# Kernel optimization log

Measured on AMD Instinct MI355X. Metric: run time of the kernel, lower is better.

The kernel has to match this reference:

```python
import jax, jax.numpy as jnp
import numpy as np

IMAGE_W = 1024
IMAGE_H = 1024
STRIDES = (8, 16, 32, 64, 128)
TOP_N = 1000
MIN_SCORE = 0.05
NMS_THR = 0.6
MAX_DET = 100
NEG = -1e9  # sentinel for suppressed scores


def _positions(stride):
    # Faithful to repo: shifts_x indexed by feature_h, shifts_y by feature_w,
    # grid built [hf, wf, 2] = [shift_x_i, shift_y_j], then permute(1,0,2).
    hf, wf = IMAGE_H // stride, IMAGE_W // stride
    sx = (jnp.arange(hf, dtype=jnp.float32) + 0.5) * stride
    sy = (jnp.arange(wf, dtype=jnp.float32) + 0.5) * stride
    pos = jnp.stack(jnp.meshgrid(sx, sy, indexing='ij'), axis=-1)  # [hf, wf, 2]
    return jnp.transpose(pos, (1, 0, 2)).reshape(-1, 2)  # [hf*wf, 2]


def _filter_level(cls_h, reg_h, ctr_h, pos):
    B, C = cls_h.shape[0], cls_h.shape[-1]
    cls_h = jax.nn.sigmoid(cls_h).reshape(B, -1, C)
    reg_h = jnp.exp(reg_h).reshape(B, -1, 4)
    ctr_h = jax.nn.sigmoid(ctr_h).reshape(B, -1)
    scores = jnp.max(cls_h, axis=-1)
    classes = jnp.argmax(cls_h, axis=-1).astype(jnp.int32)
    scores = jnp.sqrt(scores * ctr_h)
    N = scores.shape[1]
    if N >= TOP_N:
        scores, idx = jax.lax.top_k(scores, TOP_N)  # sorted descending, like torch.topk
        classes = jnp.take_along_axis(classes, idx, axis=1)
        reg_h = jnp.take_along_axis(reg_h, idx[..., None], axis=1)
        posb = pos[idx]  # [B, TOP_N, 2]
    else:
        posb = jnp.broadcast_to(pos[None], (B, N, 2))
    return scores, classes, reg_h, posb


def _snap(reg, pos):
    # reg: [B, N, 4] (l,t,r,b), pos: [B, N, 2]
    b = jnp.concatenate([pos - reg[:, :, 0:2], pos + reg[:, :, 2:4]], axis=-1)
    b = b.astype(jnp.int32)  # torch .int() truncation
    b = jnp.stack([
        jnp.maximum(b[..., 0], 0),
        jnp.maximum(b[..., 1], 0),
        jnp.minimum(b[..., 2], IMAGE_W - 1),
        jnp.minimum(b[..., 3], IMAGE_H - 1),
    ], axis=-1)
    return b.astype(jnp.float32)


def _nms_image(scores, classes, boxes):
    # scores [N], classes [N] int32, boxes [N,4] float (already snapped to int grid)
    s = jnp.where(scores > MIN_SCORE, scores, NEG)
    x1, y1, x2, y2 = boxes[:, 0], boxes[:, 1], boxes[:, 2], boxes[:, 3]
    areas = (x2 - x1) * (y2 - y1)
    out_s = -jnp.ones((MAX_DET,), jnp.float32)
    out_c = -jnp.ones((MAX_DET,), jnp.float32)
    out_b = -jnp.ones((MAX_DET, 4), jnp.float32)

    def body(i, st):
        s, os_, oc, ob = st
        idx = jnp.argmax(s)            # highest remaining score -> sorted keep order
        ok = s[idx] > MIN_SCORE        # any un-suppressed valid candidate left?
        bb = boxes[idx]
        iw = jnp.clip(jnp.minimum(x2, bb[2]) - jnp.maximum(x1, bb[0]), 0.0)
        ih = jnp.clip(jnp.minimum(y2, bb[3]) - jnp.maximum(y1, bb[1]), 0.0)
        inter = iw * ih
        iou = inter / (areas + areas[idx] - inter + 1e-12)
        s = jnp.where((iou > NMS_THR) & ok, NEG, s)
        s = s.at[idx].set(NEG)
        os_ = os_.at[i].set(jnp.where(ok, scores[idx], -1.0))
        oc = oc.at[i].set(jnp.where(ok, classes[idx].astype(jnp.float32), -1.0))
        ob = ob.at[i].set(jnp.where(ok, bb, -jnp.ones((4,), jnp.float32)))
        return (s, os_, oc, ob)

    _, os_, oc, ob = jax.lax.fori_loop(0, MAX_DET, body, (s, out_s, out_c, out_b))
    return os_, oc, ob


def _decode(cls_heads, reg_heads, ctr_heads):
    sc_l, cl_l, rg_l, ps_l = [], [], [], []
    for c, r, t, st in zip(cls_heads, reg_heads, ctr_heads, STRIDES):
        sc, cl, rg, ps = _filter_level(c, r, t, _positions(st))
        sc_l.append(sc); cl_l.append(cl); rg_l.append(rg); ps_l.append(ps)
    scores = jnp.concatenate(sc_l, axis=1)
    classes = jnp.concatenate(cl_l, axis=1)
    regs = jnp.concatenate(rg_l, axis=1)
    poss = jnp.concatenate(ps_l, axis=1)
    boxes = _snap(regs, poss)
    return jax.vmap(_nms_image)(scores, classes, boxes)


def setup_inputs() -> dict:
    key = jax.random.key(0)
    ks = jax.random.split(key, 15)
    B, C = 8, 80
    sizes = [IMAGE_H // s for s in STRIDES]
    inp = {}
    for i, hw in enumerate(sizes):
        inp[f'cls{i}'] = jax.random.normal(ks[i], (B, hw, hw, C), dtype=jnp.float32)
        # +3 so exp(reg) gives realistic ~20px extents
        inp[f'reg{i}'] = jax.random.normal(ks[5 + i], (B, hw, hw, 4), dtype=jnp.float32) + 3.0
        inp[f'ctr{i}'] = jax.random.normal(ks[10 + i], (B, hw, hw, 1), dtype=jnp.float32)
    return inp


def reference(cls0, cls1, cls2, cls3, cls4,
              reg0, reg1, reg2, reg3, reg4,
              ctr0, ctr1, ctr2, ctr3, ctr4):
    cls_heads = [cls0, cls1, cls2, cls3, cls4]
    reg_heads = [reg0, reg1, reg2, reg3, reg4]
    ctr_heads = [ctr0, ctr1, ctr2, ctr3, ctr4]
    batch_scores, batch_classes, batch_boxes = _decode(cls_heads, reg_heads, ctr_heads)
    return batch_scores, batch_classes, batch_boxes
```

## Files before the change

### kernel.cpp

```cpp
#include <hip/hip_runtime.h>

#define NPOS 21824
#define MINS 0.05f
#define BT   1024
#define NW   (BT/64)
#define TFAST 0.85f
#define CAP  16384
#define CNTSTRIDE 32

struct Ptrs { const float* cls[5]; const float* reg[5]; const float* ctr[5]; };

__device__ __forceinline__ float sigf(float x){ return 1.0f/(1.0f+expf(-x)); }

__device__ __forceinline__ unsigned long long mkkey(unsigned int b, int p){
    return ((unsigned long long)b << 16) | (unsigned)(65535 - p);
}

__device__ __forceinline__ float4 computeBox(const Ptrs& P, int img, int p){
    int base, lw, stride, lvl;
    if (p < 16384)      { lvl=0; base=0;     lw=7; stride=8;   }
    else if (p < 20480) { lvl=1; base=16384; lw=6; stride=16;  }
    else if (p < 21504) { lvl=2; base=20480; lw=5; stride=32;  }
    else if (p < 21760) { lvl=3; base=21504; lw=4; stride=64;  }
    else                { lvl=4; base=21760; lw=3; stride=128; }
    int pl = p - base;
    int h = pl >> lw, w = pl & ((1<<lw)-1);
    long long lidx = (long long)img*(1<<(2*lw)) + pl;
    float4 rg = ((const float4*)P.reg[lvl])[lidx];
    float x = (w + 0.5f)*(float)stride;
    float y = (h + 0.5f)*(float)stride;
    int ix1 = (int)(x - expf(rg.x));
    int iy1 = (int)(y - expf(rg.y));
    int ix2 = (int)(x + expf(rg.z));
    int iy2 = (int)(y + expf(rg.w));
    ix1 = max(ix1,0); iy1 = max(iy1,0);
    ix2 = min(ix2,1023); iy2 = min(iy2,1023);
    return make_float4((float)ix1,(float)iy1,(float)ix2,(float)iy2);
}

__global__ __launch_bounds__(256) void k_score(Ptrs P, float* scoreAll, int* clsAll,
                                               unsigned long long* list, int* listCnt)
{
    __shared__ int lcnt, lbase;
    int img  = blockIdx.y;
    int blk  = blockIdx.x;
    int tid  = threadIdx.x;
    int posb = tid >> 2;
    int l    = tid & 3;
    int p    = blk*64 + posb;
    int lvl, base, lw;
    if (blk < 256)      { lvl=0; base=0;     lw=7; }
    else if (blk < 320) { lvl=1; base=16384; lw=6; }
    else if (blk < 336) { lvl=2; base=20480; lw=5; }
    else if (blk < 340) { lvl=3; base=21504; lw=4; }
    else                { lvl=4; base=21760; lw=3; }
    int pl = p - base;
    long long lidx = (long long)img*(1<<(2*lw)) + pl;

    if (tid == 0) lcnt = 0;
    __syncthreads();

    const float4* c4 = (const float4*)(P.cls[lvl] + lidx*80);
    float mx = -3.4e38f; int mi = 0;
#pragma unroll
    for (int j = 0; j < 5; ++j) {
        int k = j*4 + l;
        float4 v = c4[k];
        int cb = k*4;
        if (v.x > mx){mx=v.x; mi=cb;}
        if (v.y > mx){mx=v.y; mi=cb+1;}
        if (v.z > mx){mx=v.z; mi=cb+2;}
        if (v.w > mx){mx=v.w; mi=cb+3;}
    }
#pragma unroll
    for (int d = 1; d < 4; d <<= 1) {
        float omx = __shfl_xor(mx, d);
        int   omi = __shfl_xor(mi, d);
        if (omx > mx || (omx == mx && omi < mi)) { mx = omx; mi = omi; }
    }
    int myTicket = -1;
    unsigned long long myKey = 0;
    if (l == 0) {
        float ct = P.ctr[lvl][lidx];
        float sc = sqrtf(sigf(mx)*sigf(ct));
        int o = img*NPOS + p;
        scoreAll[o] = sc;
        clsAll[o]   = mi;
        if (sc > TFAST) {
            myTicket = atomicAdd(&lcnt, 1);
            myKey = mkkey(__float_as_uint(sc), p);
        }
    }
    __syncthreads();
    if (tid == 0) lbase = lcnt ? atomicAdd(&listCnt[img*CNTSTRIDE], lcnt) : 0;
    __syncthreads();
    if (myTicket >= 0) {
        int t = lbase + myTicket;
        if (t < CAP) list[(long long)img*CAP + t] = myKey;
    }
}

__device__ void suffix_pick(const int* hist, int* wsum, int K,
                            unsigned int prefBase, int shift,
                            unsigned int* shPref, int* shK, int tid)
{
    int lo = tid*2;
    int h0 = hist[lo], h1 = hist[lo+1];
    int ls = h0 + h1;
    int lane = tid & 63, wv = tid >> 6;
    int v = ls;
#pragma unroll
    for (int off = 1; off < 64; off <<= 1) {
        int o = __shfl_down(v, off);
        if (lane + off < 64) v += o;
    }
    if (lane == 0) wsum[wv] = v;
    __syncthreads();
    int add = 0;
    for (int q = wv + 1; q < NW; ++q) add += wsum[q];
    int mine = v + add;
    int above = mine - ls;
    if (above < K && mine >= K) {
        if (above + h1 >= K) { *shPref = prefBase | ((unsigned)(lo+1) << shift); *shK = K - above; }
        else                 { *shPref = prefBase | ((unsigned)lo << shift); *shK = K - above - h1; }
    }
    __syncthreads();
}

__global__ __launch_bounds__(BT) void k_nms(Ptrs P, const float* scoreAll,
                                            const int* clsAll,
                                            const unsigned long long* list,
                                            const int* listCnt, float* out)
{
    __shared__ int histA[2048], histB[2048], wsum[NW];
    __shared__ unsigned int shPref;
    __shared__ int shK, tick, eqn;
    __shared__ unsigned long long eqKey[1024];
    __shared__ unsigned long long sel[256];
    __shared__ unsigned long long sorted[256];
    __shared__ float4 sBox[256];
    __shared__ float  sCls[256];
    __shared__ __align__(16) unsigned long long sRow[256][4];
    __shared__ int accIdx[100];
    __shared__ float4 accBox[100];
    __shared__ int shNaM, shNa;
    __shared__ unsigned long long shLast;

    int img = blockIdx.x, tid = threadIdx.x;
    const unsigned int* gs = (const unsigned int*)scoreAll + (long long)img*NPOS;
    const int* gCls = clsAll + (long long)img*NPOS;
    const unsigned long long* gl = list + (long long)img*CAP;

    float* outS = out + img*100;
    float* outC = out + 800 + img*100;
    float* outB = out + 1600 + img*400;

    int cnt = listCnt[img*CNTSTRIDE];
    bool fastPath = (cnt >= 256 && cnt <= CAP);

    for (int i = tid; i < 2048; i += BT) { histA[i] = 0; histB[i] = 0; }
    if (tid == 0) { tick = 0; eqn = 0; }
    __syncthreads();

    unsigned int kth; int need;
    if (fastPath) {
        for (int i = tid; i < cnt; i += BT)
            atomicAdd(&histA[(unsigned)(gl[i] >> 35)], 1);
        __syncthreads();
        suffix_pick(histA, wsum, 256, 0u, 19, &shPref, &shK, tid);
        unsigned int pref = shPref; int K2 = shK;
        for (int i = tid; i < cnt; i += BT) {
            unsigned long long k = gl[i];
            if ((unsigned)(k >> 35) == (pref >> 19))
                atomicAdd(&histB[(unsigned)(k >> 24) & 2047], 1);
        }
        __syncthreads();
        suffix_pick(histB, wsum, K2, pref, 8, &shPref, &shK, tid);
        kth = shPref >> 8; need = shK;
        for (int i = tid; i < cnt; i += BT) {
            unsigned long long k = gl[i];
            unsigned int hb = (unsigned)(k >> 24);
            if (hb > kth)       { int t = atomicAdd(&tick, 1); sel[t] = k; }
            else if (hb == kth) { int t = atomicAdd(&eqn, 1); if (t < 1024) eqKey[t] = k; }
        }
    } else {
#pragma unroll 4
        for (int i = tid; i < NPOS; i += BT)
            atomicAdd(&histA[gs[i] >> 19], 1);
        __syncthreads();
        suffix_pick(histA, wsum, 256, 0u, 19, &shPref, &shK, tid);
        unsigned int pref = shPref; int K2 = shK;
#pragma unroll 4
        for (int i = tid; i < NPOS; i += BT) {
            unsigned int b = gs[i];
            if ((b >> 19) == (pref >> 19)) atomicAdd(&histB[(b >> 8) & 2047], 1);
        }
        __syncthreads();
        suffix_pick(histB, wsum, K2, pref, 8, &shPref, &shK, tid);
        kth = shPref >> 8; need = shK;
#pragma unroll 4
        for (int i = tid; i < NPOS; i += BT) {
            unsigned int b = gs[i], hb = b >> 8;
            if (hb > kth)       { int t = atomicAdd(&tick, 1); sel[t] = mkkey(b, i); }
            else if (hb == kth) { int t = atomicAdd(&eqn, 1); if (t < 1024) eqKey[t] = mkkey(b, i); }
        }
    }
    __syncthreads();
    int m = eqn, nG = tick;
    if (m <= 1024) {
        for (int q = tid; q < m; q += BT) {
            unsigned long long kq = eqKey[q];
            int r = 0;
            for (int j = 0; j < m; ++j) r += (eqKey[j] > kq);
            if (r < need) sel[nG + r] = kq;
        }
    } else if (tid == 0) {
        unsigned long long last = ~0ULL;
        for (int c = 0; c < need; ++c) {
            unsigned long long best = 0;
            if (fastPath) {
                for (int i = 0; i < cnt; ++i) {
                    unsigned long long k2 = gl[i];
                    if ((unsigned)(k2 >> 24) == kth && k2 < last && k2 > best) best = k2;
                }
            } else {
                for (int i = 0; i < NPOS; ++i) {
                    unsigned int b = gs[i];
                    if ((b >> 8) == kth) {
                        unsigned long long k2 = mkkey(b, i);
                        if (k2 < last && k2 > best) best = k2;
                    }
                }
            }
            sel[nG + c] = best; last = best;
        }
    }
    __syncthreads();

    if (tid < 256) {
        unsigned long long k = sel[tid];
        int r = 0;
        for (int j = 0; j < 256; ++j) r += (sel[j] > k);
        sorted[r] = k;
    }
    __syncthreads();
    if (tid < 256) {
        int p = 65535 - (int)(sorted[tid] & 0xFFFF);
        sBox[tid] = computeBox(P, img, p);
        sCls[tid] = (float)gCls[p];
    }

    float myScore = 0.f;
    if (tid < 256) myScore = __uint_as_float((unsigned int)(sorted[tid] >> 16));
    int nValid = __syncthreads_count(myScore > MINS ? 1 : 0);

    {
        int row = tid & 255, qq = tid >> 8;
        float4 bi = sBox[row];
        float  ai = (bi.z-bi.x)*(bi.w-bi.y);
        unsigned long long mv = 0;
#pragma unroll 8
        for (int jj = 0; jj < 64; ++jj) {
            int j = qq*64 + jj;
            float4 bj = sBox[j];
            float aj = (bj.z-bj.x)*(bj.w-bj.y);
            float iw = fmaxf(fminf(bj.z,bi.z)-fmaxf(bj.x,bi.x),0.f);
            float ih = fmaxf(fminf(bj.w,bi.w)-fmaxf(bj.y,bi.y),0.f);
            float in_ = iw*ih;
            bool s = (j > row) && (in_/(aj+ai-in_+1e-12f) > 0.6f);
            mv |= ((unsigned long long)s) << jj;
        }
        sRow[row][qq] = mv;
    }
    __syncthreads();

    if (tid == 0) {
        int na = 0;
        unsigned long long r0=0, r1=0, r2=0, r3=0;
#define FCOS_WBLK(RW, IB)                                                  \
        {                                                                  \
            int hi = nValid < ((IB)+1)*64 ? nValid : ((IB)+1)*64;          \
            for (int i = (IB)*64; i < hi && na < 100; ++i) {               \
                if ((RW >> (i - (IB)*64)) & 1ull) continue;                \
                accIdx[na++] = i;                                          \
                const ulonglong2* rp = (const ulonglong2*)sRow[i];         \
                ulonglong2 ra = rp[0], rb = rp[1];                         \
                r0 |= ra.x; r1 |= ra.y; r2 |= rb.x; r3 |= rb.y;            \
            }                                                              \
        }
        FCOS_WBLK(r0,0) FCOS_WBLK(r1,1) FCOS_WBLK(r2,2) FCOS_WBLK(r3,3)
#undef FCOS_WBLK
        shNaM = na; shNa = na;
    }
    __syncthreads();

    int naM = shNaM;
    if (naM < 100 && nValid == 256) {
        if (tid < naM) accBox[tid] = sBox[accIdx[tid]];
        if (tid == 0) shLast = sorted[255];
        __syncthreads();
        while (true) {
            if (shNa >= 100) break;
            unsigned long long last = shLast;
            unsigned long long bk = 0;
            for (int i = tid; i < NPOS; i += BT) {
                unsigned long long k2 = mkkey(gs[i], i);
                if (k2 < last && k2 > bk) bk = k2;
            }
#pragma unroll
            for (int off = 32; off > 0; off >>= 1) {
                unsigned long long o = __shfl_down(bk, off);
                if (o > bk) bk = o;
            }
            int lane = tid & 63, wv = tid >> 6;
            if (lane == 0) eqKey[wv] = bk;
            __syncthreads();
            if (tid == 0) {
                unsigned long long best = 0;
                for (int q = 0; q < NW; ++q) if (eqKey[q] > best) best = eqKey[q];
                shLast = best;
            }
            __syncthreads();
            unsigned long long ck = shLast;
            if (ck == 0ULL) break;
            float sc = __uint_as_float((unsigned int)(ck >> 16));
            if (!(sc > MINS)) break;
            int p = 65535 - (int)(ck & 0xFFFF);
            float4 bb = computeBox(P, img, p);
            float ba = (bb.z-bb.x)*(bb.w-bb.y);
            int na = shNa;
            bool mySup = false;
            if (tid < na) {
                float4 ab = accBox[tid];
                float aa = (ab.z-ab.x)*(ab.w-ab.y);
                float iw = fmaxf(fminf(bb.z,ab.z)-fmaxf(bb.x,ab.x),0.f);
                float ih = fmaxf(fminf(bb.w,ab.w)-fmaxf(bb.y,ab.y),0.f);
                float in_ = iw*ih;
                mySup = in_/(ba+aa-in_+1e-12f) > 0.6f;
            }
            int supCnt = __syncthreads_count(mySup);
            if (supCnt == 0) {
                if (tid == 0) {
                    int na2 = shNa;
                    outS[na2] = sc;
                    outC[na2] = (float)gCls[p];
                    outB[4*na2+0]=bb.x; outB[4*na2+1]=bb.y;
                    outB[4*na2+2]=bb.z; outB[4*na2+3]=bb.w;
                    accBox[na2] = bb;
                    shNa = na2 + 1;
                }
            }
            __syncthreads();
        }
    }
    __syncthreads();

    {
        int naM2 = shNaM, naT = shNa;
        if (tid < 100) {
            if (tid < naM2) {
                int r = accIdx[tid];
                unsigned long long k = sorted[r];
                float4 b = sBox[r];
                outS[tid] = __uint_as_float((unsigned int)(k >> 16));
                outC[tid] = sCls[r];
                outB[4*tid+0]=b.x; outB[4*tid+1]=b.y;
                outB[4*tid+2]=b.z; outB[4*tid+3]=b.w;
            } else if (tid >= naT) {
                outS[tid] = -1.f; outC[tid] = -1.f;
                outB[4*tid+0]=-1.f; outB[4*tid+1]=-1.f;
                outB[4*tid+2]=-1.f; outB[4*tid+3]=-1.f;
            }
        }
    }
}

extern "C" void kernel_launch(void* const* d_in, const int* in_sizes, int n_in,
                              void* d_out, int out_size, void* d_ws, size_t ws_size,
                              hipStream_t stream) {
    Ptrs P;
    bool interleaved = (in_sizes[1] == 8 * 128 * 128 * 4);
    for (int i = 0; i < 5; ++i) {
        if (interleaved) {
            P.cls[i] = (const float*)d_in[3*i];
            P.reg[i] = (const float*)d_in[3*i + 1];
            P.ctr[i] = (const float*)d_in[3*i + 2];
        } else {
            P.cls[i] = (const float*)d_in[i];
            P.reg[i] = (const float*)d_in[5 + i];
            P.ctr[i] = (const float*)d_in[10 + i];
        }
    }

    char* wbase = (char*)d_ws;
    size_t off = 0;
    auto alloc = [&](size_t bytes) -> void* {
        void* r = wbase + off;
        off += (bytes + 255) & ~(size_t)255;
        return r;
    };
    float*              scoreAll = (float*)alloc((size_t)8 * NPOS * 4);
    int*                clsAll   = (int*)alloc((size_t)8 * NPOS * 4);
    unsigned long long* list     = (unsigned long long*)alloc((size_t)8 * CAP * 8);
    int*                listCnt  = (int*)alloc((size_t)8 * CNTSTRIDE * 4);

    hipMemsetAsync(listCnt, 0, 8 * CNTSTRIDE * sizeof(int), stream);

    dim3 gA(341, 8);
    k_score <<<gA, 256, 0, stream>>>(P, scoreAll, clsAll, list, listCnt);
    k_nms   <<<8, BT, 0, stream>>>(P, scoreAll, clsAll, list, listCnt, (float*)d_out);
}
```

Before: 154.0 us.

## Fuse score and NMS kernels into one cooperative kernel with grid sync

Merges the scoring kernel and the per-image NMS kernel into a single cooperative launch of 512 blocks. The blocks grid-stride over the former score blocks, then a grid-wide sync hands off to 8 blocks that run selection and NMS. This removes one kernel launch and its inter-kernel gap. In exchange the NMS phase drops from 1024 to 256 threads per block, so histogram scans, the NPOS fallback scans and the refill loop run with a quarter of the threads, and the grid sync adds its own cost.

After: 268.3 us. 1.74x slower.

```diff
diff --git a/kernel.cpp b/kernel.cpp
--- a/kernel.cpp
+++ b/kernel.cpp
@@ -1,9 +1,14 @@
 #include <hip/hip_runtime.h>
+#include <hip/hip_cooperative_groups.h>
+
+namespace cg = cooperative_groups;
 
 #define NPOS 21824
 #define MINS 0.05f
-#define BT   1024
-#define NW   (BT/64)
+#define GRID 512
+#define BT2  256
+#define NW2  4
+#define NVB  2728
 #define TFAST 0.85f
 #define CAP  16384
 #define CNTSTRIDE 32
@@ -38,75 +43,14 @@
     return make_float4((float)ix1,(float)iy1,(float)ix2,(float)iy2);
 }
 
-__global__ __launch_bounds__(256) void k_score(Ptrs P, float* scoreAll, int* clsAll,
-                                               unsigned long long* list, int* listCnt)
-{
-    __shared__ int lcnt, lbase;
-    int img  = blockIdx.y;
-    int blk  = blockIdx.x;
-    int tid  = threadIdx.x;
-    int posb = tid >> 2;
-    int l    = tid & 3;
-    int p    = blk*64 + posb;
-    int lvl, base, lw;
-    if (blk < 256)      { lvl=0; base=0;     lw=7; }
-    else if (blk < 320) { lvl=1; base=16384; lw=6; }
-    else if (blk < 336) { lvl=2; base=20480; lw=5; }
-    else if (blk < 340) { lvl=3; base=21504; lw=4; }
-    else                { lvl=4; base=21760; lw=3; }
-    int pl = p - base;
-    long long lidx = (long long)img*(1<<(2*lw)) + pl;
-
-    if (tid == 0) lcnt = 0;
-    __syncthreads();
-
-    const float4* c4 = (const float4*)(P.cls[lvl] + lidx*80);
-    float mx = -3.4e38f; int mi = 0;
-#pragma unroll
-    for (int j = 0; j < 5; ++j) {
-        int k = j*4 + l;
-        float4 v = c4[k];
-        int cb = k*4;
-        if (v.x > mx){mx=v.x; mi=cb;}
-        if (v.y > mx){mx=v.y; mi=cb+1;}
-        if (v.z > mx){mx=v.z; mi=cb+2;}
-        if (v.w > mx){mx=v.w; mi=cb+3;}
-    }
-#pragma unroll
-    for (int d = 1; d < 4; d <<= 1) {
-        float omx = __shfl_xor(mx, d);
-        int   omi = __shfl_xor(mi, d);
-        if (omx > mx || (omx == mx && omi < mi)) { mx = omx; mi = omi; }
-    }
-    int myTicket = -1;
-    unsigned long long myKey = 0;
-    if (l == 0) {
-        float ct = P.ctr[lvl][lidx];
-        float sc = sqrtf(sigf(mx)*sigf(ct));
-        int o = img*NPOS + p;
-        scoreAll[o] = sc;
-        clsAll[o]   = mi;
-        if (sc > TFAST) {
-            myTicket = atomicAdd(&lcnt, 1);
-            myKey = mkkey(__float_as_uint(sc), p);
-        }
-    }
-    __syncthreads();
-    if (tid == 0) lbase = lcnt ? atomicAdd(&listCnt[img*CNTSTRIDE], lcnt) : 0;
-    __syncthreads();
-    if (myTicket >= 0) {
-        int t = lbase + myTicket;
-        if (t < CAP) list[(long long)img*CAP + t] = myKey;
-    }
-}
-
 __device__ void suffix_pick(const int* hist, int* wsum, int K,
                             unsigned int prefBase, int shift,
                             unsigned int* shPref, int* shK, int tid)
 {
-    int lo = tid*2;
-    int h0 = hist[lo], h1 = hist[lo+1];
-    int ls = h0 + h1;
+    const int g = 2048 / BT2;
+    int lo = tid*g, ls = 0;
+#pragma unroll
+    for (int q = 0; q < g; ++q) ls += hist[lo + q];
     int lane = tid & 63, wv = tid >> 6;
     int v = ls;
 #pragma unroll
@@ -117,22 +61,28 @@
     if (lane == 0) wsum[wv] = v;
     __syncthreads();
     int add = 0;
-    for (int q = wv + 1; q < NW; ++q) add += wsum[q];
+    for (int q = wv + 1; q < NW2; ++q) add += wsum[q];
     int mine = v + add;
     int above = mine - ls;
     if (above < K && mine >= K) {
-        if (above + h1 >= K) { *shPref = prefBase | ((unsigned)(lo+1) << shift); *shK = K - above; }
-        else                 { *shPref = prefBase | ((unsigned)lo << shift); *shK = K - above - h1; }
+        int cum = above;
+        for (int b = lo + g - 1; b >= lo; --b) {
+            cum += hist[b];
+            if (cum >= K) {
+                *shPref = prefBase | ((unsigned)b << shift);
+                *shK = K - (cum - hist[b]);
+                break;
+            }
+        }
     }
     __syncthreads();
 }
 
-__global__ __launch_bounds__(BT) void k_nms(Ptrs P, const float* scoreAll,
-                                            const int* clsAll,
-                                            const unsigned long long* list,
-                                            const int* listCnt, float* out)
+__global__ __launch_bounds__(BT2) void k_fused(Ptrs P, float* scoreAll, int* clsAll,
+                                               unsigned long long* list, int* listCnt,
+                                               float* out)
 {
-    __shared__ int histA[2048], histB[2048], wsum[NW];
+    __shared__ int histA[2048], histB[2048], wsum[NW2];
     __shared__ unsigned int shPref;
     __shared__ int shK, tick, eqn;
     __shared__ unsigned long long eqKey[1024];
@@ -145,8 +95,72 @@
     __shared__ float4 accBox[100];
     __shared__ int shNaM, shNa;
     __shared__ unsigned long long shLast;
-
-    int img = blockIdx.x, tid = threadIdx.x;
+    __shared__ int lcnt, lbase;
+
+    int tid = threadIdx.x;
+
+    for (int vb = blockIdx.x; vb < NVB; vb += GRID) {
+        int img = vb / 341;
+        int blk = vb - img*341;
+        int posb = tid >> 2;
+        int l    = tid & 3;
+        int p    = blk*64 + posb;
+        int lvl, base, lw;
+        if (blk < 256)      { lvl=0; base=0;     lw=7; }
+        else if (blk < 320) { lvl=1; base=16384; lw=6; }
+        else if (blk < 336) { lvl=2; base=20480; lw=5; }
+        else if (blk < 340) { lvl=3; base=21504; lw=4; }
+        else                { lvl=4; base=21760; lw=3; }
+        int pl = p - base;
+        long long lidx = (long long)img*(1<<(2*lw)) + pl;
+
+        if (tid == 0) lcnt = 0;
+        __syncthreads();
+
+        const float4* c4 = (const float4*)(P.cls[lvl] + lidx*80);
+        float mx = -3.4e38f; int mi = 0;
+#pragma unroll
+        for (int j = 0; j < 5; ++j) {
+            int k = j*4 + l;
+            float4 v = c4[k];
+            int cb = k*4;
+            if (v.x > mx){mx=v.x; mi=cb;}
+            if (v.y > mx){mx=v.y; mi=cb+1;}
+            if (v.z > mx){mx=v.z; mi=cb+2;}
+            if (v.w > mx){mx=v.w; mi=cb+3;}
+        }
+#pragma unroll
+        for (int d = 1; d < 4; d <<= 1) {
+            float omx = __shfl_xor(mx, d);
+            int   omi = __shfl_xor(mi, d);
+            if (omx > mx || (omx == mx && omi < mi)) { mx = omx; mi = omi; }
+        }
+        int myTicket = -1;
+        unsigned long long myKey = 0;
+        if (l == 0) {
+            float ct = P.ctr[lvl][lidx];
+            float sc = sqrtf(sigf(mx)*sigf(ct));
+            int o = img*NPOS + p;
+            scoreAll[o] = sc;
+            clsAll[o]   = mi;
+            if (sc > TFAST) {
+                myTicket = atomicAdd(&lcnt, 1);
+                myKey = mkkey(__float_as_uint(sc), p);
+            }
+        }
+        __syncthreads();
+        if (tid == 0) lbase = lcnt ? atomicAdd(&listCnt[img*CNTSTRIDE], lcnt) : 0;
+        __syncthreads();
+        if (myTicket >= 0) {
+            int t = lbase + myTicket;
+            if (t < CAP) list[(long long)img*CAP + t] = myKey;
+        }
+    }
+
+    cg::this_grid().sync();
+
+    if (blockIdx.x >= 8) return;
+    int img = blockIdx.x;
     const unsigned int* gs = (const unsigned int*)scoreAll + (long long)img*NPOS;
     const int* gCls = clsAll + (long long)img*NPOS;
     const unsigned long long* gl = list + (long long)img*CAP;
@@ -158,18 +172,18 @@
     int cnt = listCnt[img*CNTSTRIDE];
     bool fastPath = (cnt >= 256 && cnt <= CAP);
 
-    for (int i = tid; i < 2048; i += BT) { histA[i] = 0; histB[i] = 0; }
+    for (int i = tid; i < 2048; i += BT2) { histA[i] = 0; histB[i] = 0; }
     if (tid == 0) { tick = 0; eqn = 0; }
     __syncthreads();
 
     unsigned int kth; int need;
     if (fastPath) {
-        for (int i = tid; i < cnt; i += BT)
+        for (int i = tid; i < cnt; i += BT2)
             atomicAdd(&histA[(unsigned)(gl[i] >> 35)], 1);
         __syncthreads();
         suffix_pick(histA, wsum, 256, 0u, 19, &shPref, &shK, tid);
         unsigned int pref = shPref; int K2 = shK;
-        for (int i = tid; i < cnt; i += BT) {
+        for (int i = tid; i < cnt; i += BT2) {
             unsigned long long k = gl[i];
             if ((unsigned)(k >> 35) == (pref >> 19))
                 atomicAdd(&histB[(unsigned)(k >> 24) & 2047], 1);
@@ -177,7 +191,7 @@
         __syncthreads();
         suffix_pick(histB, wsum, K2, pref, 8, &shPref, &shK, tid);
         kth = shPref >> 8; need = shK;
-        for (int i = tid; i < cnt; i += BT) {
+        for (int i = tid; i < cnt; i += BT2) {
             unsigned long long k = gl[i];
             unsigned int hb = (unsigned)(k >> 24);
             if (hb > kth)       { int t = atomicAdd(&tick, 1); sel[t] = k; }
@@ -185,13 +199,13 @@
         }
     } else {
 #pragma unroll 4
-        for (int i = tid; i < NPOS; i += BT)
+        for (int i = tid; i < NPOS; i += BT2)
             atomicAdd(&histA[gs[i] >> 19], 1);
         __syncthreads();
         suffix_pick(histA, wsum, 256, 0u, 19, &shPref, &shK, tid);
         unsigned int pref = shPref; int K2 = shK;
 #pragma unroll 4
-        for (int i = tid; i < NPOS; i += BT) {
+        for (int i = tid; i < NPOS; i += BT2) {
             unsigned int b = gs[i];
             if ((b >> 19) == (pref >> 19)) atomicAdd(&histB[(b >> 8) & 2047], 1);
         }
@@ -199,7 +213,7 @@
         suffix_pick(histB, wsum, K2, pref, 8, &shPref, &shK, tid);
         kth = shPref >> 8; need = shK;
 #pragma unroll 4
-        for (int i = tid; i < NPOS; i += BT) {
+        for (int i = tid; i < NPOS; i += BT2) {
             unsigned int b = gs[i], hb = b >> 8;
             if (hb > kth)       { int t = atomicAdd(&tick, 1); sel[t] = mkkey(b, i); }
             else if (hb == kth) { int t = atomicAdd(&eqn, 1); if (t < 1024) eqKey[t] = mkkey(b, i); }
@@ -208,7 +222,7 @@
     __syncthreads();
     int m = eqn, nG = tick;
     if (m <= 1024) {
-        for (int q = tid; q < m; q += BT) {
+        for (int q = tid; q < m; q += BT2) {
             unsigned long long kq = eqKey[q];
             int r = 0;
             for (int j = 0; j < m; ++j) r += (eqKey[j] > kq);
@@ -237,40 +251,41 @@
     }
     __syncthreads();
 
-    if (tid < 256) {
+    {
         unsigned long long k = sel[tid];
         int r = 0;
         for (int j = 0; j < 256; ++j) r += (sel[j] > k);
         sorted[r] = k;
     }
     __syncthreads();
-    if (tid < 256) {
+    {
         int p = 65535 - (int)(sorted[tid] & 0xFFFF);
         sBox[tid] = computeBox(P, img, p);
         sCls[tid] = (float)gCls[p];
     }
 
-    float myScore = 0.f;
-    if (tid < 256) myScore = __uint_as_float((unsigned int)(sorted[tid] >> 16));
+    float myScore = __uint_as_float((unsigned int)(sorted[tid] >> 16));
     int nValid = __syncthreads_count(myScore > MINS ? 1 : 0);
 
     {
-        int row = tid & 255, qq = tid >> 8;
-        float4 bi = sBox[row];
+        float4 bi = sBox[tid];
         float  ai = (bi.z-bi.x)*(bi.w-bi.y);
-        unsigned long long mv = 0;
+#pragma unroll
+        for (int qq = 0; qq < 4; ++qq) {
+            unsigned long long mv = 0;
 #pragma unroll 8
-        for (int jj = 0; jj < 64; ++jj) {
-            int j = qq*64 + jj;
-            float4 bj = sBox[j];
-            float aj = (bj.z-bj.x)*(bj.w-bj.y);
-            float iw = fmaxf(fminf(bj.z,bi.z)-fmaxf(bj.x,bi.x),0.f);
-            float ih = fmaxf(fminf(bj.w,bi.w)-fmaxf(bj.y,bi.y),0.f);
-            float in_ = iw*ih;
-            bool s = (j > row) && (in_/(aj+ai-in_+1e-12f) > 0.6f);
-            mv |= ((unsigned long long)s) << jj;
-        }
-        sRow[row][qq] = mv;
+            for (int jj = 0; jj < 64; ++jj) {
+                int j = qq*64 + jj;
+                float4 bj = sBox[j];
+                float aj = (bj.z-bj.x)*(bj.w-bj.y);
+                float iw = fmaxf(fminf(bj.z,bi.z)-fmaxf(bj.x,bi.x),0.f);
+                float ih = fmaxf(fminf(bj.w,bi.w)-fmaxf(bj.y,bi.y),0.f);
+                float in_ = iw*ih;
+                bool s = (j > tid) && (in_/(aj+ai-in_+1e-12f) > 0.6f);
+                mv |= ((unsigned long long)s) << jj;
+            }
+            sRow[tid][qq] = mv;
+        }
     }
     __syncthreads();
 
@@ -303,7 +318,7 @@
             if (shNa >= 100) break;
             unsigned long long last = shLast;
             unsigned long long bk = 0;
-            for (int i = tid; i < NPOS; i += BT) {
+            for (int i = tid; i < NPOS; i += BT2) {
                 unsigned long long k2 = mkkey(gs[i], i);
                 if (k2 < last && k2 > bk) bk = k2;
             }
@@ -317,7 +332,7 @@
             __syncthreads();
             if (tid == 0) {
                 unsigned long long best = 0;
-                for (int q = 0; q < NW; ++q) if (eqKey[q] > best) best = eqKey[q];
+                for (int q = 0; q < NW2; ++q) if (eqKey[q] > best) best = eqKey[q];
                 shLast = best;
             }
             __syncthreads();
@@ -406,7 +421,9 @@
 
     hipMemsetAsync(listCnt, 0, 8 * CNTSTRIDE * sizeof(int), stream);
 
-    dim3 gA(341, 8);
-    k_score <<<gA, 256, 0, stream>>>(P, scoreAll, clsAll, list, listCnt);
-    k_nms   <<<8, BT, 0, stream>>>(P, scoreAll, clsAll, list, listCnt, (float*)d_out);
+    float* outF = (float*)d_out;
+    void* args[] = { (void*)&P, (void*)&scoreAll, (void*)&clsAll,
+                     (void*)&list, (void*)&listCnt, (void*)&outF };
+    hipLaunchCooperativeKernel((const void*)k_fused, dim3(GRID), dim3(BT2),
+                               args, 0, stream);
 }
```
